# Optimization experiments

Hardware: AMD Instinct MI355X
Metric: run time of the kernel (lower is better)

Reference implementation:

```python
import jax, jax.numpy as jnp
import numpy as np

NUM_USER = 1_000_000
NUM_ITEM = 100_000
HIDDEN = 64
NUM_PAIRS = 2_000_000


def setup_inputs() -> dict:
    key = jax.random.key(0)
    k1, k2, k3, k4 = jax.random.split(key, 4)
    user_emb = jax.random.normal(k1, (NUM_USER, HIDDEN), dtype=jnp.float32)
    item_emb = jax.random.normal(k2, (NUM_ITEM, HIDDEN), dtype=jnp.float32)
    user_ids = jax.random.randint(k3, (NUM_PAIRS,), 0, NUM_USER, dtype=jnp.int32)
    item_ids = jax.random.randint(k4, (NUM_PAIRS,), 0, NUM_ITEM, dtype=jnp.int32)
    return {"user_emb": user_emb, "item_emb": item_emb,
            "user_ids": user_ids, "item_ids": item_ids}


def reference(user_emb, item_emb, user_ids, item_ids):
    # PMF rating prediction: relu(<U[u], V[i]>) for each observed (u, i) pair.
    u = user_emb[user_ids]          # [P, D] gather
    v = item_emb[item_ids]          # [P, D] gather
    ratings = jnp.einsum('pd,pd->p', u, v)  # per-pair dot product
    return jax.nn.relu(ratings)
```

## Files before the change

### kernel.cpp

```cpp
#include <hip/hip_runtime.h>
#include <stdint.h>


constexpr int HIDDEN = 64;
constexpr int K      = 4;
constexpr int NB     = 512;
constexpr int BSHIFT = 11;
constexpr int PPB    = 8192;

__device__ __forceinline__ float dot16(const float4& a, const float4& b) {
    return a.x * b.x + a.y * b.y + a.z * b.z + a.w * b.w;
}

__device__ __forceinline__ uint64_t pack_pair(int uid, int iid, int pos) {
    return ((uint64_t)uid << 38) | ((uint64_t)iid << 21) | (uint64_t)pos;
}

__global__ __launch_bounds__(256) void hist_kernel(
    const int* __restrict__ user_ids, int* __restrict__ ghist, int n)
{
    __shared__ int h[NB];
    for (int i = threadIdx.x; i < NB; i += 256) h[i] = 0;
    __syncthreads();
    const int base = blockIdx.x * PPB;
    for (int i = threadIdx.x; i < PPB; i += 256) {
        int p = base + i;
        if (p < n) atomicAdd(&h[user_ids[p] >> BSHIFT], 1);
    }
    __syncthreads();
    for (int i = threadIdx.x; i < NB; i += 256) {
        int c = h[i];
        if (c) atomicAdd(&ghist[i], c);
    }
}

__global__ __launch_bounds__(512) void scan_kernel(
    const int* __restrict__ ghist, int* __restrict__ cursor)
{
    __shared__ int s[NB];
    const int t = threadIdx.x;
    int v = ghist[t];
    s[t] = v;
    __syncthreads();
    #pragma unroll
    for (int d = 1; d < NB; d <<= 1) {
        int x = (t >= d) ? s[t - d] : 0;
        __syncthreads();
        s[t] += x;
        __syncthreads();
    }
    cursor[t] = s[t] - v;
}

__global__ __launch_bounds__(256) void scatter_kernel(
    const int* __restrict__ user_ids, const int* __restrict__ item_ids,
    int* __restrict__ cursor, uint64_t* __restrict__ sorted, int n)
{
    __shared__ int h[NB];
    __shared__ int gbase[NB];
    for (int i = threadIdx.x; i < NB; i += 256) h[i] = 0;
    __syncthreads();
    const int base = blockIdx.x * PPB;
    for (int i = threadIdx.x; i < PPB; i += 256) {
        int p = base + i;
        if (p < n) atomicAdd(&h[user_ids[p] >> BSHIFT], 1);
    }
    __syncthreads();
    for (int i = threadIdx.x; i < NB; i += 256) {
        int c = h[i];
        gbase[i] = c ? atomicAdd(&cursor[i], c) : 0;
    }
    __syncthreads();
    for (int i = threadIdx.x; i < NB; i += 256) h[i] = 0;
    __syncthreads();
    for (int i = threadIdx.x; i < PPB; i += 256) {
        int p = base + i;
        if (p < n) {
            int u = user_ids[p];
            int b = u >> BSHIFT;
            int r = atomicAdd(&h[b], 1);
            sorted[(size_t)gbase[b] + r] = pack_pair(u, item_ids[p], p);
        }
    }
}

__global__ __launch_bounds__(256) void pmf_dot_sorted(
    const float* __restrict__ user_emb, const float* __restrict__ item_emb,
    const uint64_t* __restrict__ sorted, float* __restrict__ out,
    int n, int chunk)
{
    const int b2     = (blockIdx.x & 7) * chunk + (blockIdx.x >> 3);
    const int group  = b2 * 16 + (threadIdx.x >> 4);
    const int lane16 = threadIdx.x & 15;
    const int q0     = group * K;

    if (q0 + K <= n) {
        const ulonglong2 v01 = *reinterpret_cast<const ulonglong2*>(sorted + q0);
        const ulonglong2 v23 = *reinterpret_cast<const ulonglong2*>(sorted + q0 + 2);
        const uint64_t v0 = v01.x, v1 = v01.y, v2 = v23.x, v3 = v23.y;

        const int u0 = (int)(v0 >> 38), i0 = (int)((v0 >> 21) & 0x1FFFF), p0 = (int)(v0 & 0x1FFFFF);
        const int u1 = (int)(v1 >> 38), i1 = (int)((v1 >> 21) & 0x1FFFF), p1 = (int)(v1 & 0x1FFFFF);
        const int u2 = (int)(v2 >> 38), i2 = (int)((v2 >> 21) & 0x1FFFF), p2 = (int)(v2 & 0x1FFFFF);
        const int u3 = (int)(v3 >> 38), i3 = (int)((v3 >> 21) & 0x1FFFF), p3 = (int)(v3 & 0x1FFFFF);

        const float4 a0 = *(reinterpret_cast<const float4*>(user_emb + (size_t)u0 * HIDDEN) + lane16);
        const float4 a1 = *(reinterpret_cast<const float4*>(user_emb + (size_t)u1 * HIDDEN) + lane16);
        const float4 a2 = *(reinterpret_cast<const float4*>(user_emb + (size_t)u2 * HIDDEN) + lane16);
        const float4 a3 = *(reinterpret_cast<const float4*>(user_emb + (size_t)u3 * HIDDEN) + lane16);
        const float4 b0 = *(reinterpret_cast<const float4*>(item_emb + (size_t)i0 * HIDDEN) + lane16);
        const float4 b1 = *(reinterpret_cast<const float4*>(item_emb + (size_t)i1 * HIDDEN) + lane16);
        const float4 b2v = *(reinterpret_cast<const float4*>(item_emb + (size_t)i2 * HIDDEN) + lane16);
        const float4 b3 = *(reinterpret_cast<const float4*>(item_emb + (size_t)i3 * HIDDEN) + lane16);

        float d0 = dot16(a0, b0);
        float d1 = dot16(a1, b1);
        float d2 = dot16(a2, b2v);
        float d3 = dot16(a3, b3);

        #pragma unroll
        for (int s = 1; s < 16; s <<= 1) {
            d0 += __shfl_xor(d0, s, 16);
            d1 += __shfl_xor(d1, s, 16);
            d2 += __shfl_xor(d2, s, 16);
            d3 += __shfl_xor(d3, s, 16);
        }

        if (lane16 == 0) {
            out[p0] = d0 > 0.0f ? d0 : 0.0f;
            out[p1] = d1 > 0.0f ? d1 : 0.0f;
            out[p2] = d2 > 0.0f ? d2 : 0.0f;
            out[p3] = d3 > 0.0f ? d3 : 0.0f;
        }
    } else if (q0 < n) {
        for (int q = q0; q < n; ++q) {
            const uint64_t v = sorted[q];
            const int u = (int)(v >> 38), i = (int)((v >> 21) & 0x1FFFF), p = (int)(v & 0x1FFFFF);
            const float4 a = *(reinterpret_cast<const float4*>(user_emb + (size_t)u * HIDDEN) + lane16);
            const float4 b = *(reinterpret_cast<const float4*>(item_emb + (size_t)i * HIDDEN) + lane16);
            float d = dot16(a, b);
            #pragma unroll
            for (int s = 1; s < 16; s <<= 1) d += __shfl_xor(d, s, 16);
            if (lane16 == 0) out[p] = d > 0.0f ? d : 0.0f;
        }
    }
}

__global__ __launch_bounds__(256) void pmf_dot_direct(
    const float* __restrict__ user_emb, const float* __restrict__ item_emb,
    const int* __restrict__ user_ids, const int* __restrict__ item_ids,
    float* __restrict__ out, int n)
{
    const int group  = (blockIdx.x * blockDim.x + threadIdx.x) >> 4;
    const int lane16 = threadIdx.x & 15;
    const int p0     = group * K;
    if (p0 + K <= n) {
        const int4 u4 = *reinterpret_cast<const int4*>(user_ids + p0);
        const int4 i4 = *reinterpret_cast<const int4*>(item_ids + p0);
        const float4 a0 = *(reinterpret_cast<const float4*>(user_emb + (size_t)u4.x * HIDDEN) + lane16);
        const float4 a1 = *(reinterpret_cast<const float4*>(user_emb + (size_t)u4.y * HIDDEN) + lane16);
        const float4 a2 = *(reinterpret_cast<const float4*>(user_emb + (size_t)u4.z * HIDDEN) + lane16);
        const float4 a3 = *(reinterpret_cast<const float4*>(user_emb + (size_t)u4.w * HIDDEN) + lane16);
        const float4 b0 = *(reinterpret_cast<const float4*>(item_emb + (size_t)i4.x * HIDDEN) + lane16);
        const float4 b1 = *(reinterpret_cast<const float4*>(item_emb + (size_t)i4.y * HIDDEN) + lane16);
        const float4 b2 = *(reinterpret_cast<const float4*>(item_emb + (size_t)i4.z * HIDDEN) + lane16);
        const float4 b3 = *(reinterpret_cast<const float4*>(item_emb + (size_t)i4.w * HIDDEN) + lane16);
        float d0 = dot16(a0, b0), d1 = dot16(a1, b1), d2 = dot16(a2, b2), d3 = dot16(a3, b3);
        #pragma unroll
        for (int s = 1; s < 16; s <<= 1) {
            d0 += __shfl_xor(d0, s, 16);
            d1 += __shfl_xor(d1, s, 16);
            d2 += __shfl_xor(d2, s, 16);
            d3 += __shfl_xor(d3, s, 16);
        }
        if (lane16 == 0) {
            float4 r = { d0 > 0.0f ? d0 : 0.0f, d1 > 0.0f ? d1 : 0.0f,
                         d2 > 0.0f ? d2 : 0.0f, d3 > 0.0f ? d3 : 0.0f };
            *reinterpret_cast<float4*>(out + p0) = r;
        }
    } else if (p0 < n) {
        for (int p = p0; p < n; ++p) {
            const int uid = user_ids[p];
            const int iid = item_ids[p];
            const float4 a = *(reinterpret_cast<const float4*>(user_emb + (size_t)uid * HIDDEN) + lane16);
            const float4 b = *(reinterpret_cast<const float4*>(item_emb + (size_t)iid * HIDDEN) + lane16);
            float d = dot16(a, b);
            #pragma unroll
            for (int s = 1; s < 16; s <<= 1) d += __shfl_xor(d, s, 16);
            if (lane16 == 0) out[p] = d > 0.0f ? d : 0.0f;
        }
    }
}

extern "C" void kernel_launch(void* const* d_in, const int* in_sizes, int n_in,
                              void* d_out, int out_size, void* d_ws, size_t ws_size,
                              hipStream_t stream) {
    const float* user_emb = (const float*)d_in[0];
    const float* item_emb = (const float*)d_in[1];
    const int*   user_ids = (const int*)d_in[2];
    const int*   item_ids = (const int*)d_in[3];
    float* out = (float*)d_out;

    const int n = in_sizes[2];

    const size_t sortedOff = 4096;
    const size_t need = sortedOff + (size_t)n * 8;

    const int threads = 256;
    const int pairs_per_dot_block = (threads / 16) * K;
    int dot_blocks = (n + pairs_per_dot_block - 1) / pairs_per_dot_block;

    if (ws_size >= need) {
        char* ws = (char*)d_ws;
        int*      ghist  = (int*)ws;
        int*      cursor = (int*)(ws + NB * 4);
        uint64_t* sorted = (uint64_t*)(ws + sortedOff);

        hipMemsetAsync(ghist, 0, NB * 4, stream);

        const int part_blocks = (n + PPB - 1) / PPB;
        hist_kernel<<<part_blocks, threads, 0, stream>>>(user_ids, ghist, n);
        scan_kernel<<<1, NB, 0, stream>>>(ghist, cursor);
        scatter_kernel<<<part_blocks, threads, 0, stream>>>(
            user_ids, item_ids, cursor, sorted, n);

        const int blocks8 = ((dot_blocks + 7) / 8) * 8;
        const int chunk   = blocks8 / 8;
        pmf_dot_sorted<<<blocks8, threads, 0, stream>>>(
            user_emb, item_emb, sorted, out, n, chunk);
    } else {
        pmf_dot_direct<<<dot_blocks, threads, 0, stream>>>(
            user_emb, item_emb, user_ids, item_ids, out, n);
    }
}
```

Measured before the change: 494.2 us.

## Switch bucket sort to finer buckets with direct global atomics

Raises the bucket count from 512 to 8192, so each bucket covers 128 users instead of 2048. The histogram and scatter kernels drop their shared-memory per-block histograms and use one global atomicAdd per pair into a grid-stride loop. The scan now handles 8192 entries, with each of 1024 threads doing eight. Finer buckets give better gather locality in the dot kernel, but the scatter no longer writes bucket-contiguous runs per block, and global atomic contention on cursors grows.

After: 580.5 us. 1.17x slower.

```diff
diff --git a/kernel.cpp b/kernel.cpp
--- a/kernel.cpp
+++ b/kernel.cpp
@@ -4,9 +4,8 @@
 
 constexpr int HIDDEN = 64;
 constexpr int K      = 4;
-constexpr int NB     = 512;
-constexpr int BSHIFT = 11;
-constexpr int PPB    = 8192;
+constexpr int NB     = 8192;
+constexpr int BSHIFT = 7;
 
 __device__ __forceinline__ float dot16(const float4& a, const float4& b) {
     return a.x * b.x + a.y * b.y + a.z * b.z + a.w * b.w;
@@ -19,68 +18,49 @@
 __global__ __launch_bounds__(256) void hist_kernel(
     const int* __restrict__ user_ids, int* __restrict__ ghist, int n)
 {
-    __shared__ int h[NB];
-    for (int i = threadIdx.x; i < NB; i += 256) h[i] = 0;
-    __syncthreads();
-    const int base = blockIdx.x * PPB;
-    for (int i = threadIdx.x; i < PPB; i += 256) {
-        int p = base + i;
-        if (p < n) atomicAdd(&h[user_ids[p] >> BSHIFT], 1);
-    }
-    __syncthreads();
-    for (int i = threadIdx.x; i < NB; i += 256) {
-        int c = h[i];
-        if (c) atomicAdd(&ghist[i], c);
-    }
-}
-
-__global__ __launch_bounds__(512) void scan_kernel(
+    const int stride = gridDim.x * blockDim.x;
+    for (int p = blockIdx.x * blockDim.x + threadIdx.x; p < n; p += stride)
+        atomicAdd(&ghist[user_ids[p] >> BSHIFT], 1);
+}
+
+__global__ __launch_bounds__(1024) void scan_kernel(
     const int* __restrict__ ghist, int* __restrict__ cursor)
 {
-    __shared__ int s[NB];
+    __shared__ int part[1024];
     const int t = threadIdx.x;
-    int v = ghist[t];
-    s[t] = v;
+    int v[8];
+    int4 h0 = reinterpret_cast<const int4*>(ghist)[t * 2];
+    int4 h1 = reinterpret_cast<const int4*>(ghist)[t * 2 + 1];
+    v[0] = h0.x; v[1] = h0.y; v[2] = h0.z; v[3] = h0.w;
+    v[4] = h1.x; v[5] = h1.y; v[6] = h1.z; v[7] = h1.w;
+    int sum = 0;
+    #pragma unroll
+    for (int i = 0; i < 8; ++i) { int x = v[i]; v[i] = sum; sum += x; }
+    part[t] = sum;
     __syncthreads();
     #pragma unroll
-    for (int d = 1; d < NB; d <<= 1) {
-        int x = (t >= d) ? s[t - d] : 0;
+    for (int d = 1; d < 1024; d <<= 1) {
+        int x = (t >= d) ? part[t - d] : 0;
         __syncthreads();
-        s[t] += x;
+        part[t] += x;
         __syncthreads();
     }
-    cursor[t] = s[t] - v;
+    const int base = part[t] - sum;
+    int4 o0 = { v[0] + base, v[1] + base, v[2] + base, v[3] + base };
+    int4 o1 = { v[4] + base, v[5] + base, v[6] + base, v[7] + base };
+    reinterpret_cast<int4*>(cursor)[t * 2]     = o0;
+    reinterpret_cast<int4*>(cursor)[t * 2 + 1] = o1;
 }
 
 __global__ __launch_bounds__(256) void scatter_kernel(
     const int* __restrict__ user_ids, const int* __restrict__ item_ids,
     int* __restrict__ cursor, uint64_t* __restrict__ sorted, int n)
 {
-    __shared__ int h[NB];
-    __shared__ int gbase[NB];
-    for (int i = threadIdx.x; i < NB; i += 256) h[i] = 0;
-    __syncthreads();
-    const int base = blockIdx.x * PPB;
-    for (int i = threadIdx.x; i < PPB; i += 256) {
-        int p = base + i;
-        if (p < n) atomicAdd(&h[user_ids[p] >> BSHIFT], 1);
-    }
-    __syncthreads();
-    for (int i = threadIdx.x; i < NB; i += 256) {
-        int c = h[i];
-        gbase[i] = c ? atomicAdd(&cursor[i], c) : 0;
-    }
-    __syncthreads();
-    for (int i = threadIdx.x; i < NB; i += 256) h[i] = 0;
-    __syncthreads();
-    for (int i = threadIdx.x; i < PPB; i += 256) {
-        int p = base + i;
-        if (p < n) {
-            int u = user_ids[p];
-            int b = u >> BSHIFT;
-            int r = atomicAdd(&h[b], 1);
-            sorted[(size_t)gbase[b] + r] = pack_pair(u, item_ids[p], p);
-        }
+    const int stride = gridDim.x * blockDim.x;
+    for (int p = blockIdx.x * blockDim.x + threadIdx.x; p < n; p += stride) {
+        int u = user_ids[p];
+        int q = atomicAdd(&cursor[u >> BSHIFT], 1);
+        sorted[q] = pack_pair(u, item_ids[p], p);
     }
 }
 
@@ -203,8 +183,8 @@
 
     const int n = in_sizes[2];
 
-    const size_t sortedOff = 4096;
-    const size_t need = sortedOff + (size_t)n * 8;
+    const size_t sortedOff = (size_t)2 * NB * 4;
+    const size_t need      = sortedOff + (size_t)n * 8;
 
     const int threads = 256;
     const int pairs_per_dot_block = (threads / 16) * K;
@@ -218,10 +198,10 @@
 
         hipMemsetAsync(ghist, 0, NB * 4, stream);
 
-        const int part_blocks = (n + PPB - 1) / PPB;
-        hist_kernel<<<part_blocks, threads, 0, stream>>>(user_ids, ghist, n);
-        scan_kernel<<<1, NB, 0, stream>>>(ghist, cursor);
-        scatter_kernel<<<part_blocks, threads, 0, stream>>>(
+        const int lin_blocks = 2048;
+        hist_kernel<<<lin_blocks, threads, 0, stream>>>(user_ids, ghist, n);
+        scan_kernel<<<1, 1024, 0, stream>>>(ghist, cursor);
+        scatter_kernel<<<lin_blocks, threads, 0, stream>>>(
             user_ids, item_ids, cursor, sorted, n);
 
         const int blocks8 = ((dot_blocks + 7) / 8) * 8;
```
